# Kernel tuning notes

Measured on AMD Instinct MI355X. Metric: run time of the kernel, lower is better.

## Reference

```python
import jax, jax.numpy as jnp
import numpy as np

NEG_SLOPE = 0.2
N_NODES = 50000


def _gat_layer(x, src, dst, invalid, W, al, ar, b):
    # x: [N, Fin]; src/dst: [E] (self-loops appended); invalid: [E] bool
    N = x.shape[0]
    H, F = al.shape
    z = (x @ W).reshape(N, H, F)                       # [N,H,F]
    el = jnp.sum(z * al[None], axis=-1)                # [N,H]
    er = jnp.sum(z * ar[None], axis=-1)                # [N,H]
    e = el[src] + er[dst]                              # [E,H]
    e = jnp.where(e > 0, e, NEG_SLOPE * e)             # LeakyReLU(0.2)
    e = jnp.where(invalid[:, None], -jnp.inf, e)       # removed self-loop edges
    # edge softmax per destination node (every node has a self-loop -> max finite)
    m = jax.ops.segment_max(e, dst, num_segments=N)    # [N,H]
    ex = jnp.exp(e - m[dst])
    ex = jnp.where(invalid[:, None], 0.0, ex)
    s = jax.ops.segment_sum(ex, dst, num_segments=N)   # [N,H]
    alpha = ex / s[dst]                                # [E,H]
    msg = z[src] * alpha[:, :, None]                   # [E,H,F]
    out = jax.ops.segment_sum(msg, dst, num_segments=N)  # [N,H,F]
    out = out + b.reshape(1, H, F)
    return jax.nn.elu(out)


def _with_self_loops(src, dst):
    N = N_NODES
    loop = jnp.arange(N, dtype=src.dtype)
    invalid = jnp.concatenate([src == dst, jnp.zeros(N, dtype=bool)])
    return jnp.concatenate([src, loop]), jnp.concatenate([dst, loop]), invalid


def setup_inputs() -> dict:
    key = jax.random.key(0)
    ks = jax.random.split(key, 12)
    N, Fin, H0, F0, H1, C = N_NODES, 256, 4, 32, 1, 40
    E = 800000
    sc = lambda k, shp, fan: jax.random.normal(k, shp, jnp.float32) * (1.0 / np.sqrt(fan))
    return {
        "x": jax.random.normal(ks[0], (N, Fin), jnp.float32),
        "src": jax.random.randint(ks[1], (E,), 0, N, jnp.int32),
        "dst": jax.random.randint(ks[2], (E,), 0, N, jnp.int32),
        "W0": sc(ks[3], (Fin, H0 * F0), Fin),
        "al0": sc(ks[4], (H0, F0), F0),
        "ar0": sc(ks[5], (H0, F0), F0),
        "b0": jnp.zeros((H0 * F0,), jnp.float32),
        "W1": sc(ks[6], (H0 * F0, H1 * C), H0 * F0),
        "al1": sc(ks[7], (H1, C), C),
        "ar1": sc(ks[8], (H1, C), C),
        "b1": jnp.zeros((C,), jnp.float32),
    }


def reference(x, src, dst, W0, al0, ar0, b0, W1, al1, ar1, b1):
    s, d, invalid = _with_self_loops(src, dst)
    h = _gat_layer(x, s, d, invalid, W0, al0, ar0, b0)   # [N,4,32]
    h = h.reshape(h.shape[0], -1)                        # flatten(1) -> [N,128]
    h = _gat_layer(h, s, d, invalid, W1, al1, ar1, b1)   # [N,1,40]
    return h.mean(axis=1)                                # mean over heads -> [N,40]
```

## Files before the change

kernel.cpp:

```cpp
#include <hip/hip_runtime.h>
#include <stdint.h>

#define NN 50000
#define EE 800000
#define CAP 48
#define NXCD 8
#define NPX 6250
#define EPB 2048
#define NCHUNK 391
#define GB0 782

typedef __bf16 bf16x8 __attribute__((ext_vector_type(8)));
typedef float  f32x4  __attribute__((ext_vector_type(4)));

__device__ __forceinline__ float bflo(unsigned int w){ union{unsigned int i;float f;}c; c.i=w<<16; return c.f; }
__device__ __forceinline__ float bfhi(unsigned int w){ union{unsigned int i;float f;}c; c.i=w&0xFFFF0000u; return c.f; }
__device__ __forceinline__ bf16x8 bf8_zero(){
  bf16x8 v;
  #pragma unroll
  for (int j=0;j<8;++j) v[j]=(__bf16)0.f;
  return v;
}

__global__ __launch_bounds__(256) void k_prep(const float* __restrict__ W0,
                                              __bf16* __restrict__ Wg,
                                              int* __restrict__ cursor,
                                              int* __restrict__ csrv){
  int tg = blockIdx.x*256 + threadIdx.x;
  if (tg < 4096){
    int k8 = tg >> 7, n = tg & 127;
    bf16x8 v;
    #pragma unroll
    for (int j=0;j<8;++j) v[j] = (__bf16)W0[(k8*8+j)*128 + n];
    *(bf16x8*)(Wg + ((size_t)(k8*128 + n))*8) = v;
  }
  if (tg < NN){
    cursor[tg] = 1;
    csrv[(size_t)tg*CAP] = tg;
  }
}

__global__ __launch_bounds__(256) void k_gemm0_scatter(const float* __restrict__ x,
    const __bf16* __restrict__ Wg, const float* __restrict__ al0, const float* __restrict__ ar0,
    __bf16* __restrict__ z0b, float* __restrict__ el0, float* __restrict__ er0,
    const int* __restrict__ src, const int* __restrict__ dst,
    int* __restrict__ cursor, int* __restrict__ csrv){
  if (blockIdx.x >= GB0){
    const int xcd = blockIdx.x & 7;
    const int chunk = (blockIdx.x - GB0) >> 3;
    const int lo = xcd*NPX, hi = lo + NPX;
    int e = chunk*EPB + threadIdx.x;
    #pragma unroll
    for (int it=0; it<EPB/256; ++it, e += 256){
      if (e < EE){
        int d = dst[e];
        if (d >= lo && d < hi){
          int s = src[e];
          unsigned int inv = (s==d) ? 0x80000000u : 0u;
          int pos = atomicAdd(&cursor[d], 1);
          csrv[(size_t)d*CAP + pos] = (int)((unsigned int)s | inv);
        }
      }
    }
    return;
  }
  const int tid = threadIdx.x;
  const int wv = tid >> 6, ln = tid & 63, q = ln >> 4, mr = ln & 15;
  const int nhalf = wv & 1, mhalf = wv >> 1;
  const int m0w = blockIdx.x*64 + mhalf*32;
  const int n0w = nhalf*64;
  f32x4 acc[2][4];
  #pragma unroll
  for (int mt=0;mt<2;++mt)
    #pragma unroll
    for (int nt=0;nt<4;++nt) acc[mt][nt] = (f32x4){0.f,0.f,0.f,0.f};
  const bool av0 = (m0w + mr) < NN;
  const bool av1 = (m0w + 16 + mr) < NN;
  const float* xr0 = x + (size_t)(m0w + mr)*256;
  const float* xr1 = x + (size_t)(m0w + 16 + mr)*256;
  #pragma unroll
  for (int kc=0;kc<8;++kc){
    int ko = kc*32 + q*8;
    bf16x8 a0 = bf8_zero(), a1 = bf8_zero();
    if (av0){
      float4 p = *(const float4*)(xr0 + ko);
      float4 p2 = *(const float4*)(xr0 + ko + 4);
      a0[0]=(__bf16)p.x; a0[1]=(__bf16)p.y; a0[2]=(__bf16)p.z; a0[3]=(__bf16)p.w;
      a0[4]=(__bf16)p2.x; a0[5]=(__bf16)p2.y; a0[6]=(__bf16)p2.z; a0[7]=(__bf16)p2.w;
    }
    if (av1){
      float4 p = *(const float4*)(xr1 + ko);
      float4 p2 = *(const float4*)(xr1 + ko + 4);
      a1[0]=(__bf16)p.x; a1[1]=(__bf16)p.y; a1[2]=(__bf16)p.z; a1[3]=(__bf16)p.w;
      a1[4]=(__bf16)p2.x; a1[5]=(__bf16)p2.y; a1[6]=(__bf16)p2.z; a1[7]=(__bf16)p2.w;
    }
    const __bf16* wb = Wg + ((size_t)((kc*4+q)*128 + n0w + mr))*8;
    #pragma unroll
    for (int nt=0;nt<4;++nt){
      bf16x8 bf = *(const bf16x8*)(wb + (size_t)nt*16*8);
      acc[0][nt] = __builtin_amdgcn_mfma_f32_16x16x32_bf16(a0, bf, acc[0][nt], 0,0,0);
      acc[1][nt] = __builtin_amdgcn_mfma_f32_16x16x32_bf16(a1, bf, acc[1][nt], 0,0,0);
    }
  }
  float alv[4], arv[4];
  #pragma unroll
  for (int nt=0;nt<4;++nt){ int c = n0w + nt*16 + mr; alv[nt]=al0[c]; arv[nt]=ar0[c]; }
  #pragma unroll
  for (int mt=0;mt<2;++mt){
    #pragma unroll
    for (int r=0;r<4;++r){
      int grow = m0w + mt*16 + q*4 + r;
      if (grow < NN){
        #pragma unroll
        for (int nt=0;nt<4;++nt)
          z0b[(size_t)grow*128 + n0w + nt*16 + mr] = (__bf16)acc[mt][nt][r];
      }
      float pl0 = acc[mt][0][r]*alv[0] + acc[mt][1][r]*alv[1];
      float pr0 = acc[mt][0][r]*arv[0] + acc[mt][1][r]*arv[1];
      float pl1 = acc[mt][2][r]*alv[2] + acc[mt][3][r]*alv[3];
      float pr1 = acc[mt][2][r]*arv[2] + acc[mt][3][r]*arv[3];
      #pragma unroll
      for (int off=1; off<16; off<<=1){
        pl0 += __shfl_xor(pl0, off, 16); pr0 += __shfl_xor(pr0, off, 16);
        pl1 += __shfl_xor(pl1, off, 16); pr1 += __shfl_xor(pr1, off, 16);
      }
      if (mr==0 && grow<NN){
        el0[grow*4 + 2*nhalf]   = pl0; er0[grow*4 + 2*nhalf]   = pr0;
        el0[grow*4 + 2*nhalf+1] = pl1; er0[grow*4 + 2*nhalf+1] = pr1;
      }
    }
  }
}

__global__ __launch_bounds__(256) void k_agg0(const unsigned short* __restrict__ z0b,
    const float* __restrict__ el0, const float* __restrict__ er0,
    const int* __restrict__ cursor, const int* __restrict__ csrv,
    const float* __restrict__ b0, unsigned short* __restrict__ hb){
  int lane = threadIdx.x & 63;
  int i = __builtin_amdgcn_readfirstlane(blockIdx.x*4 + (threadIdx.x >> 6));
  int h1 = lane >> 4;
  int lane2 = lane << 1;
  const float erv = er0[(size_t)i*4 + h1];
  float ax=0.f, ay=0.f, s=0.f;
  int p = i*CAP, pe = p + cursor[i];
  for (; p+8<=pe; p+=8){
    int4 va = *(const int4*)(csrv + p);
    int4 vb = *(const int4*)(csrv + p + 4);
    int v[8] = {va.x,va.y,va.z,va.w,vb.x,vb.y,vb.z,vb.w};
    float el[8];
    #pragma unroll
    for (int j=0;j<8;++j) el[j] = el0[(size_t)(v[j]&0x7FFFFFFF)*4 + h1];
    unsigned int zw[8];
    #pragma unroll
    for (int j=0;j<8;++j)
      zw[j] = *(const unsigned int*)(z0b + (size_t)(v[j]&0x7FFFFFFF)*128 + lane2);
    #pragma unroll
    for (int j=0;j<8;++j){
      float e = el[j] + erv;
      e = fmaxf(e, 0.2f*e);
      float w = (v[j] < 0) ? 0.f : __expf(e);
      s += w; ax = fmaf(w, bflo(zw[j]), ax); ay = fmaf(w, bfhi(zw[j]), ay);
    }
  }
  for (; p+4<=pe; p+=4){
    int4 va = *(const int4*)(csrv + p);
    int v[4] = {va.x,va.y,va.z,va.w};
    float el[4];
    #pragma unroll
    for (int j=0;j<4;++j) el[j] = el0[(size_t)(v[j]&0x7FFFFFFF)*4 + h1];
    unsigned int zw[4];
    #pragma unroll
    for (int j=0;j<4;++j)
      zw[j] = *(const unsigned int*)(z0b + (size_t)(v[j]&0x7FFFFFFF)*128 + lane2);
    #pragma unroll
    for (int j=0;j<4;++j){
      float e = el[j] + erv;
      e = fmaxf(e, 0.2f*e);
      float w = (v[j] < 0) ? 0.f : __expf(e);
      s += w; ax = fmaf(w, bflo(zw[j]), ax); ay = fmaf(w, bfhi(zw[j]), ay);
    }
  }
  for (; p<pe; ++p){
    int v = csrv[p];
    int u = v & 0x7FFFFFFF;
    float e = el0[(size_t)u*4 + h1] + erv;
    e = fmaxf(e, 0.2f*e);
    float w = (v < 0) ? 0.f : __expf(e);
    unsigned int zw = *(const unsigned int*)(z0b + (size_t)u*128 + lane2);
    s += w; ax = fmaf(w, bflo(zw), ax); ay = fmaf(w, bfhi(zw), ay);
  }
  float inv = 1.f/s;
  float ox = ax*inv + b0[lane*2], oy = ay*inv + b0[lane*2+1];
  ox = ox>0.f?ox:__expf(ox)-1.f; oy = oy>0.f?oy:__expf(oy)-1.f;
  union { __bf16 b[2]; unsigned int u; } pk;
  pk.b[0]=(__bf16)ox; pk.b[1]=(__bf16)oy;
  *(unsigned int*)(hb + (size_t)i*128 + lane2) = pk.u;
}

__global__ __launch_bounds__(256) void k_gemm1(const __bf16* __restrict__ hb,
    const float* __restrict__ W1, const float* __restrict__ al1, const float* __restrict__ ar1,
    __bf16* __restrict__ z1b, float* __restrict__ el1, float* __restrict__ er1){
  __shared__ __bf16 Blds[16][48][8];
  const int tid = threadIdx.x;
  for (int t=tid; t<16*48*8; t+=256) (&Blds[0][0][0])[t] = (__bf16)0.f;
  __syncthreads();
  for (int t=tid; t<5120; t+=256){
    int k = t/40, n = t - k*40;
    Blds[k>>3][n][k&7] = (__bf16)W1[t];
  }
  __syncthreads();
  const int wm = tid >> 6, ln = tid & 63, q = ln >> 4, mr = ln & 15;
  const int m0 = blockIdx.x*64 + wm*16;
  const int arow = m0 + mr;
  const bool av = (arow < NN);
  f32x4 acc[3];
  #pragma unroll
  for (int nt=0;nt<3;++nt) acc[nt] = (f32x4){0.f,0.f,0.f,0.f};
  #pragma unroll
  for (int kc=0;kc<4;++kc){
    bf16x8 af = bf8_zero();
    if (av) af = *(const bf16x8*)(hb + (size_t)arow*128 + kc*32 + q*8);
    #pragma unroll
    for (int nt=0;nt<3;++nt){
      bf16x8 bf = *(const bf16x8*)&Blds[kc*4+q][nt*16+mr][0];
      acc[nt] = __builtin_amdgcn_mfma_f32_16x16x32_bf16(af, bf, acc[nt], 0,0,0);
    }
  }
  float alv[3], arv[3];
  #pragma unroll
  for (int nt=0;nt<3;++nt){
    int c = nt*16+mr;
    alv[nt] = (c<40) ? al1[c] : 0.f;
    arv[nt] = (c<40) ? ar1[c] : 0.f;
  }
  #pragma unroll
  for (int r=0;r<4;++r){
    int grow = m0 + q*4 + r;
    if (grow < NN){
      #pragma unroll
      for (int nt=0;nt<3;++nt){
        int c = nt*16+mr;
        if (c < 40) z1b[(size_t)grow*40 + c] = (__bf16)acc[nt][r];
      }
    }
    float pl = acc[0][r]*alv[0] + acc[1][r]*alv[1] + acc[2][r]*alv[2];
    float pr = acc[0][r]*arv[0] + acc[1][r]*arv[1] + acc[2][r]*arv[2];
    #pragma unroll
    for (int off=1; off<16; off<<=1){ pl += __shfl_xor(pl, off, 16); pr += __shfl_xor(pr, off, 16); }
    if (mr==0 && grow<NN){ el1[grow]=pl; er1[grow]=pr; }
  }
}

__global__ __launch_bounds__(256) void k_agg1(const unsigned short* __restrict__ z1b,
    const float* __restrict__ el1, const float* __restrict__ er1,
    const int* __restrict__ cursor, const int* __restrict__ csrv,
    const float* __restrict__ b1, float* __restrict__ out){
  int lane = threadIdx.x & 63;
  int i = __builtin_amdgcn_readfirstlane(blockIdx.x*4 + (threadIdx.x >> 6));
  int fl = (lane < 20) ? (lane<<1) : 0;
  const float erv = er1[i];
  float ax=0.f, ay=0.f, s=0.f;
  int p = i*CAP, pe = p + cursor[i];
  for (; p+8<=pe; p+=8){
    int4 va = *(const int4*)(csrv + p);
    int4 vb = *(const int4*)(csrv + p + 4);
    int v[8] = {va.x,va.y,va.z,va.w,vb.x,vb.y,vb.z,vb.w};
    float el[8];
    #pragma unroll
    for (int j=0;j<8;++j) el[j] = el1[v[j]&0x7FFFFFFF];
    unsigned int zw[8];
    #pragma unroll
    for (int j=0;j<8;++j)
      zw[j] = *(const unsigned int*)(z1b + (size_t)(v[j]&0x7FFFFFFF)*40 + fl);
    #pragma unroll
    for (int j=0;j<8;++j){
      float e = el[j] + erv;
      e = fmaxf(e, 0.2f*e);
      float w = (v[j] < 0) ? 0.f : __expf(e);
      s += w; ax = fmaf(w, bflo(zw[j]), ax); ay = fmaf(w, bfhi(zw[j]), ay);
    }
  }
  for (; p+4<=pe; p+=4){
    int4 va = *(const int4*)(csrv + p);
    int v[4] = {va.x,va.y,va.z,va.w};
    float el[4];
    #pragma unroll
    for (int j=0;j<4;++j) el[j] = el1[v[j]&0x7FFFFFFF];
    unsigned int zw[4];
    #pragma unroll
    for (int j=0;j<4;++j)
      zw[j] = *(const unsigned int*)(z1b + (size_t)(v[j]&0x7FFFFFFF)*40 + fl);
    #pragma unroll
    for (int j=0;j<4;++j){
      float e = el[j] + erv;
      e = fmaxf(e, 0.2f*e);
      float w = (v[j] < 0) ? 0.f : __expf(e);
      s += w; ax = fmaf(w, bflo(zw[j]), ax); ay = fmaf(w, bfhi(zw[j]), ay);
    }
  }
  for (; p<pe; ++p){
    int v = csrv[p];
    int u = v & 0x7FFFFFFF;
    float e = el1[u] + erv;
    e = fmaxf(e, 0.2f*e);
    float w = (v < 0) ? 0.f : __expf(e);
    unsigned int zw = *(const unsigned int*)(z1b + (size_t)u*40 + fl);
    s += w; ax = fmaf(w, bflo(zw), ax); ay = fmaf(w, bfhi(zw), ay);
  }
  if (lane < 20){
    float inv = 1.f/s;
    float ox = ax*inv + b1[lane*2], oy = ay*inv + b1[lane*2+1];
    ox = ox>0.f?ox:__expf(ox)-1.f; oy = oy>0.f?oy:__expf(oy)-1.f;
    *(float2*)(out + (size_t)i*40 + (lane<<1)) = make_float2(ox, oy);
  }
}

extern "C" void kernel_launch(void* const* d_in, const int* in_sizes, int n_in,
                              void* d_out, int out_size, void* d_ws, size_t ws_size,
                              hipStream_t stream){
  const float* x   = (const float*)d_in[0];
  const int*   src = (const int*)d_in[1];
  const int*   dst = (const int*)d_in[2];
  const float* W0  = (const float*)d_in[3];
  const float* al0 = (const float*)d_in[4];
  const float* ar0 = (const float*)d_in[5];
  const float* b0  = (const float*)d_in[6];
  const float* W1  = (const float*)d_in[7];
  const float* al1 = (const float*)d_in[8];
  const float* ar1 = (const float*)d_in[9];
  const float* b1  = (const float*)d_in[10];
  float* out = (float*)d_out;

  __bf16* z0b = (__bf16*)d_ws;
  __bf16* hb  = z0b + (size_t)NN*128;
  __bf16* z1b = hb  + (size_t)NN*128;
  __bf16* Wg  = z1b + (size_t)NN*40;
  float* el0 = (float*)(Wg + 32768);
  float* er0 = el0 + (size_t)NN*4;
  float* el1 = er0 + (size_t)NN*4;
  float* er1 = el1 + NN;
  int* cursor = (int*)(er1 + NN);
  int* csrv   = cursor + NN;

  k_prep<<<(NN+255)/256, 256, 0, stream>>>(W0, Wg, cursor, csrv);
  k_gemm0_scatter<<<GB0 + NCHUNK*NXCD, 256, 0, stream>>>(x, Wg, al0, ar0, z0b, el0, er0,
                                                         src, dst, cursor, csrv);
  k_agg0 <<<NN/4, 256, 0, stream>>>((const unsigned short*)z0b, el0, er0, cursor, csrv, b0, (unsigned short*)hb);
  k_gemm1<<<(NN+63)/64, 256, 0, stream>>>(hb, W1, al1, ar1, z1b, el1, er1);
  k_agg1 <<<NN/4, 256, 0, stream>>>((const unsigned short*)z1b, el1, er1, cursor, csrv, b1, out);
}
```

Measured before the change: 225.8 us.

## Replace XCD-partitioned edge scatter with single-pass vectorized scatter placed first

The edge-to-CSR scatter used to have every XCD re-read all edges and keep only destinations in its node range, so the src/dst arrays were read eight times in total. Now each edge is read once with int4 vector loads (8 edges per thread), and the scatter blocks come before the GEMM blocks in the grid. This cuts edge-read traffic and the block count, but the atomics on cursor and the csrv writes are no longer confined to one XCD's L2 slice, which may cost cross-die coherence traffic.

```diff
diff --git a/kernel.cpp b/kernel.cpp
--- a/kernel.cpp
+++ b/kernel.cpp
@@ -4,10 +4,7 @@
 #define NN 50000
 #define EE 800000
 #define CAP 48
-#define NXCD 8
-#define NPX 6250
-#define EPB 2048
-#define NCHUNK 391
+#define SCB 391
 #define GB0 782
 
 typedef __bf16 bf16x8 __attribute__((ext_vector_type(8)));
@@ -45,21 +42,21 @@
     __bf16* __restrict__ z0b, float* __restrict__ el0, float* __restrict__ er0,
     const int* __restrict__ src, const int* __restrict__ dst,
     int* __restrict__ cursor, int* __restrict__ csrv){
-  if (blockIdx.x >= GB0){
-    const int xcd = blockIdx.x & 7;
-    const int chunk = (blockIdx.x - GB0) >> 3;
-    const int lo = xcd*NPX, hi = lo + NPX;
-    int e = chunk*EPB + threadIdx.x;
-    #pragma unroll
-    for (int it=0; it<EPB/256; ++it, e += 256){
-      if (e < EE){
-        int d = dst[e];
-        if (d >= lo && d < hi){
-          int s = src[e];
-          unsigned int inv = (s==d) ? 0x80000000u : 0u;
-          int pos = atomicAdd(&cursor[d], 1);
-          csrv[(size_t)d*CAP + pos] = (int)((unsigned int)s | inv);
-        }
+  if (blockIdx.x < SCB){
+    int t = (blockIdx.x*256 + threadIdx.x) * 8;
+    if (t < EE){
+      int4 da = *(const int4*)(dst + t);
+      int4 db = *(const int4*)(dst + t + 4);
+      int4 sa = *(const int4*)(src + t);
+      int4 sb = *(const int4*)(src + t + 4);
+      int dv[8] = {da.x,da.y,da.z,da.w,db.x,db.y,db.z,db.w};
+      int sv[8] = {sa.x,sa.y,sa.z,sa.w,sb.x,sb.y,sb.z,sb.w};
+      #pragma unroll
+      for (int j=0;j<8;++j){
+        int d = dv[j], s = sv[j];
+        unsigned int inv = (s==d) ? 0x80000000u : 0u;
+        int pos = atomicAdd(&cursor[d], 1);
+        csrv[(size_t)d*CAP + pos] = (int)((unsigned int)s | inv);
       }
     }
     return;
@@ -67,7 +64,7 @@
   const int tid = threadIdx.x;
   const int wv = tid >> 6, ln = tid & 63, q = ln >> 4, mr = ln & 15;
   const int nhalf = wv & 1, mhalf = wv >> 1;
-  const int m0w = blockIdx.x*64 + mhalf*32;
+  const int m0w = (blockIdx.x - SCB)*64 + mhalf*32;
   const int n0w = nhalf*64;
   f32x4 acc[2][4];
   #pragma unroll
@@ -343,8 +340,8 @@
   int* csrv   = cursor + NN;
 
   k_prep<<<(NN+255)/256, 256, 0, stream>>>(W0, Wg, cursor, csrv);
-  k_gemm0_scatter<<<GB0 + NCHUNK*NXCD, 256, 0, stream>>>(x, Wg, al0, ar0, z0b, el0, er0,
-                                                         src, dst, cursor, csrv);
+  k_gemm0_scatter<<<SCB + GB0, 256, 0, stream>>>(x, Wg, al0, ar0, z0b, el0, er0,
+                                                 src, dst, cursor, csrv);
   k_agg0 <<<NN/4, 256, 0, stream>>>((const unsigned short*)z0b, el0, er0, cursor, csrv, b0, (unsigned short*)hb);
   k_gemm1<<<(NN+63)/64, 256, 0, stream>>>(hb, W1, al1, ar1, z1b, el1, er1);
   k_agg1 <<<NN/4, 256, 0, stream>>>((const unsigned short*)z1b, el1, er1, cursor, csrv, b1, out);
```

Result: slower. 235.4 us (+4.2%).
